# Kernel tuning notes

Hardware: AMD Instinct MI355X
Metric: run time of the kernel (lower is better)

The kernel has to match this reference:

```python
import jax, jax.numpy as jnp
import numpy as np

B, N, C = 32, 3136, 512
H = W = 56           # h = w = sqrt(n)
NUM_HEADS = 8
HEAD_DIM = C // NUM_HEADS
AGENT_NUM = 49
POOL = 7             # int(sqrt(agent_num))
SCALE = HEAD_DIM ** -0.5


def setup_inputs() -> dict:
    key = jax.random.key(0)
    ks = jax.random.split(key, 6)
    return {
        "x": jax.random.normal(ks[0], (B, N, C), dtype=jnp.float32),
        "qkv_w": jax.random.normal(ks[1], (3 * C, C), dtype=jnp.float32) * 0.02,
        "proj_w": jax.random.normal(ks[2], (C, C), dtype=jnp.float32) * 0.02,
        "proj_b": jax.random.normal(ks[3], (C,), dtype=jnp.float32) * 0.02,
        "dwc_w": jax.random.normal(ks[4], (C, 1, 3, 3), dtype=jnp.float32) * 0.02,
        "dwc_b": jax.random.normal(ks[5], (C,), dtype=jnp.float32) * 0.02,
    }


def reference(x, qkv_w, proj_w, proj_b, dwc_w, dwc_b):
    b, n, c = x.shape
    # qkv projection (no bias)
    qkv = jnp.einsum('bnc,dc->bnd', x, qkv_w).reshape(b, n, 3, c)
    q, k, v = qkv[:, :, 0], qkv[:, :, 1], qkv[:, :, 2]  # each (b, n, c)

    # adaptive avg pool q -> agent tokens (b, agent_num, c); 56/7 = stride 8
    s = H // POOL
    agent = q.reshape(b, POOL, s, POOL, s, c).mean(axis=(2, 4)).reshape(b, AGENT_NUM, c)

    # split heads: (b, heads, seq, head_dim)
    qh = q.reshape(b, n, NUM_HEADS, HEAD_DIM).transpose(0, 2, 1, 3)
    kh = k.reshape(b, n, NUM_HEADS, HEAD_DIM).transpose(0, 2, 1, 3)
    vh = v.reshape(b, n, NUM_HEADS, HEAD_DIM).transpose(0, 2, 1, 3)
    ah = agent.reshape(b, AGENT_NUM, NUM_HEADS, HEAD_DIM).transpose(0, 2, 1, 3)

    # agent aggregation: softmax((agent*scale) @ k^T) @ v -> (b, h, agent, d)
    agent_attn = jax.nn.softmax(jnp.einsum('bhad,bhnd->bhan', ah * SCALE, kh), axis=-1)
    agent_v = jnp.einsum('bhan,bhnd->bhad', agent_attn, vh)

    # query broadcast: softmax((q*scale) @ agent^T) @ agent_v -> (b, h, n, d)
    q_attn = jax.nn.softmax(jnp.einsum('bhnd,bhad->bhna', qh * SCALE, ah), axis=-1)
    out = jnp.einsum('bhna,bhad->bhnd', q_attn, agent_v)
    out = out.transpose(0, 2, 1, 3).reshape(b, n, c)

    # depthwise conv residual on v (NCHW)
    v_img = v.reshape(b, H, W, c).transpose(0, 3, 1, 2)
    dwc = jax.lax.conv_general_dilated(
        v_img, dwc_w, window_strides=(1, 1), padding=((1, 1), (1, 1)),
        dimension_numbers=('NCHW', 'OIHW', 'NCHW'), feature_group_count=c)
    dwc = dwc + dwc_b[None, :, None, None]
    out = out + dwc.transpose(0, 2, 3, 1).reshape(b, n, c)

    # output projection
    return jnp.einsum('bnc,dc->bnd', out, proj_w) + proj_b
```

## Files before the change

### kernel.cpp

```cpp
#include <hip/hip_runtime.h>

#define B_SZ 32
#define N_TOK 3136
#define C_DIM 512
#define H_IMG 56
#define NUM_HEADS 8
#define HEAD_DIM 64
#define AGENT_NUM 49
#define SCALE 0.125f
#define M_ROWS (B_SZ * N_TOK)
#define N_SPLIT 7

typedef __bf16 bf16x8 __attribute__((ext_vector_type(8)));
typedef float f32x4 __attribute__((ext_vector_type(4)));
typedef unsigned short u16x8 __attribute__((ext_vector_type(8)));
typedef unsigned int u32x4 __attribute__((ext_vector_type(4)));

static __device__ __forceinline__ unsigned short f2bf(float f) {
    unsigned int u = __float_as_uint(f);
    unsigned int r = (u + 0x7fffu + ((u >> 16) & 1u)) >> 16;
    return (unsigned short)r;
}
static __device__ __forceinline__ float bf2f(unsigned short u) {
    return __uint_as_float(((unsigned int)u) << 16);
}
static __device__ __forceinline__ void load_lds16(const unsigned short* g, unsigned short* l) {
    __builtin_amdgcn_global_load_lds(
        (const __attribute__((address_space(1))) unsigned int*)g,
        (__attribute__((address_space(3))) unsigned int*)l, 16, 0, 0);
}

__global__ __launch_bounds__(256) void cast_f32_bf16(
    const float* __restrict__ in, unsigned short* __restrict__ out)
{
    long i = (long)blockIdx.x * 256 + threadIdx.x;
    float4 f = ((const float4*)in)[i];
    ushort4 u;
    u.x = f2bf(f.x); u.y = f2bf(f.y); u.z = f2bf(f.z); u.w = f2bf(f.w);
    ((ushort4*)out)[i] = u;
}

__global__ __launch_bounds__(256) void mfma_qkv_bf(
    const unsigned short* __restrict__ Ab, const unsigned short* __restrict__ Wb,
    float* __restrict__ qO, unsigned short* __restrict__ kO,
    unsigned short* __restrict__ vO)
{
    __shared__ __align__(16) unsigned short Asm[2][128 * 32];
    __shared__ __align__(16) unsigned short Bsm[2][128 * 32];

    const int NWG  = (M_ROWS / 128) * 12;
    const int PERX = NWG >> 3;
    const int bid = blockIdx.x;
    const int l = (bid & 7) * PERX + (bid >> 3);
    const int m0 = (l / 12) * 128, n0 = (l % 12) * 128;

    const int tid = threadIdx.x;
    const int lane = tid & 63, wave = tid >> 6;
    const int wm = wave >> 1, wn = wave & 1;

    f32x4 acc[4][4];
#pragma unroll
    for (int i = 0; i < 4; i++)
#pragma unroll
        for (int j = 0; j < 4; j++) {
            f32x4 z = {0.f, 0.f, 0.f, 0.f};
            acc[i][j] = z;
        }

    const unsigned short* aP0 = Ab + (long)(m0 + (tid >> 2)) * 512 + (tid & 3) * 8;
    const unsigned short* aP1 = aP0 + (long)64 * 512;
    const unsigned short* bP0 = Wb + (long)(n0 + (tid >> 2)) * 512 + (tid & 3) * 8;
    const unsigned short* bP1 = bP0 + (long)64 * 512;
    const int stA0 = wave * 512;
    const int stA1 = wave * 512 + 2048;

    const int fr = lane & 15, fq = lane >> 4;
    const int fOff = fq * 8;

    load_lds16(aP0, Asm[0] + stA0);
    load_lds16(aP1, Asm[0] + stA1);
    load_lds16(bP0, Bsm[0] + stA0);
    load_lds16(bP1, Bsm[0] + stA1);
    __syncthreads();

    int cur = 0;
    for (int step = 0; step < 16; ++step) {
        if (step < 15) {
            const int k0 = (step + 1) * 32;
            load_lds16(aP0 + k0, Asm[cur ^ 1] + stA0);
            load_lds16(aP1 + k0, Asm[cur ^ 1] + stA1);
            load_lds16(bP0 + k0, Bsm[cur ^ 1] + stA0);
            load_lds16(bP1 + k0, Bsm[cur ^ 1] + stA1);
        }
        const unsigned short* aF = Asm[cur] + (wm * 64 + fr) * 32 + fOff;
        const unsigned short* bF = Bsm[cur] + (wn * 64 + fr) * 32 + fOff;
        bf16x8 af[4], bfr[4];
#pragma unroll
        for (int i = 0; i < 4; i++) af[i]  = *(const bf16x8*)(aF + i * 16 * 32);
#pragma unroll
        for (int j = 0; j < 4; j++) bfr[j] = *(const bf16x8*)(bF + j * 16 * 32);
#pragma unroll
        for (int i = 0; i < 4; i++)
#pragma unroll
            for (int j = 0; j < 4; j++)
                acc[i][j] = __builtin_amdgcn_mfma_f32_16x16x32_bf16(
                    af[i], bfr[j], acc[i][j], 0, 0, 0);
        __syncthreads();
        cur ^= 1;
    }

    const int seg = n0 >> 9;
#pragma unroll
    for (int i = 0; i < 4; i++) {
        int rbase = m0 + wm * 64 + i * 16 + fq * 4;
#pragma unroll
        for (int j = 0; j < 4; j++) {
            int col  = n0 + wn * 64 + j * 16 + fr;
            int nloc = col - seg * 512;
#pragma unroll
            for (int r = 0; r < 4; r++) {
                long m = rbase + r;
                float val = acc[i][j][r];
                if (seg == 0)      qO[m * 512 + nloc] = val;
                else if (seg == 1) kO[m * 512 + nloc] = f2bf(val);
                else               vO[m * 512 + nloc] = f2bf(val);
            }
        }
    }
}

__global__ __launch_bounds__(256) void mfma_qkv(
    const float* __restrict__ A, const unsigned short* __restrict__ Wb,
    float* __restrict__ qO, unsigned short* __restrict__ kO,
    unsigned short* __restrict__ vO)
{
    __shared__ __align__(16) unsigned short Asm[128 * 32];
    __shared__ __align__(16) unsigned short Bsm[128 * 32];

    const int m0 = blockIdx.x * 128, n0 = blockIdx.y * 128;
    const int tid = threadIdx.x;
    const int lane = tid & 63, wave = tid >> 6;
    const int wm = wave >> 1, wn = wave & 1;

    f32x4 acc[4][4];
#pragma unroll
    for (int i = 0; i < 4; i++)
#pragma unroll
        for (int j = 0; j < 4; j++) {
            f32x4 z = {0.f, 0.f, 0.f, 0.f};
            acc[i][j] = z;
        }

    const int arow = tid >> 1, acol = (tid & 1) * 16;
    const float* aP = A + (long)(m0 + arow) * 512 + acol;
    unsigned short* aD = Asm + arow * 32 + acol;

    const unsigned short* bP0 = Wb + (long)(n0 + (tid >> 2)) * 512 + (tid & 3) * 8;
    const unsigned short* bP1 = bP0 + (long)64 * 512;
    unsigned short* bD0 = Bsm + (tid >> 6) * 512;
    unsigned short* bD1 = bD0 + 4 * 512;

    const int fr = lane & 15, fq = lane >> 4;
    const unsigned short* aF = Asm + (wm * 64 + fr) * 32 + fq * 8;
    const unsigned short* bF = Bsm + (wn * 64 + fr) * 32 + fq * 8;

    for (int k0 = 0; k0 < 512; k0 += 32) {
        load_lds16(bP0 + k0, bD0);
        load_lds16(bP1 + k0, bD1);
        float4 f0 = *(const float4*)(aP + k0 + 0);
        float4 f1 = *(const float4*)(aP + k0 + 4);
        float4 f2 = *(const float4*)(aP + k0 + 8);
        float4 f3 = *(const float4*)(aP + k0 + 12);
        ushort4 u0, u1, u2, u3;
        u0.x = f2bf(f0.x); u0.y = f2bf(f0.y); u0.z = f2bf(f0.z); u0.w = f2bf(f0.w);
        u1.x = f2bf(f1.x); u1.y = f2bf(f1.y); u1.z = f2bf(f1.z); u1.w = f2bf(f1.w);
        u2.x = f2bf(f2.x); u2.y = f2bf(f2.y); u2.z = f2bf(f2.z); u2.w = f2bf(f2.w);
        u3.x = f2bf(f3.x); u3.y = f2bf(f3.y); u3.z = f2bf(f3.z); u3.w = f2bf(f3.w);
        *(ushort4*)(aD + 0)  = u0;
        *(ushort4*)(aD + 4)  = u1;
        *(ushort4*)(aD + 8)  = u2;
        *(ushort4*)(aD + 12) = u3;
        __syncthreads();

        bf16x8 af[4], bfr[4];
#pragma unroll
        for (int i = 0; i < 4; i++) af[i]  = *(const bf16x8*)(aF + i * 16 * 32);
#pragma unroll
        for (int j = 0; j < 4; j++) bfr[j] = *(const bf16x8*)(bF + j * 16 * 32);
#pragma unroll
        for (int i = 0; i < 4; i++)
#pragma unroll
            for (int j = 0; j < 4; j++)
                acc[i][j] = __builtin_amdgcn_mfma_f32_16x16x32_bf16(
                    af[i], bfr[j], acc[i][j], 0, 0, 0);
        __syncthreads();
    }

    const int seg = n0 >> 9;
#pragma unroll
    for (int i = 0; i < 4; i++) {
        int rbase = m0 + wm * 64 + i * 16 + fq * 4;
#pragma unroll
        for (int j = 0; j < 4; j++) {
            int col  = n0 + wn * 64 + j * 16 + fr;
            int nloc = col - seg * 512;
#pragma unroll
            for (int r = 0; r < 4; r++) {
                long m = rbase + r;
                float val = acc[i][j][r];
                if (seg == 0)      qO[m * 512 + nloc] = val;
                else if (seg == 1) kO[m * 512 + nloc] = f2bf(val);
                else               vO[m * 512 + nloc] = f2bf(val);
            }
        }
    }
}

__global__ __launch_bounds__(256) void mfma_proj(
    const unsigned short* __restrict__ Ab, const unsigned short* __restrict__ Wb,
    const float* __restrict__ bias, float* __restrict__ C)
{
    __shared__ __align__(16) unsigned short Asm[2][128 * 32];
    __shared__ __align__(16) unsigned short Bsm[2][128 * 32];

    const int NWG  = (M_ROWS / 128) * 4;
    const int PERX = NWG >> 3;
    const int bid = blockIdx.x;
    const int l = (bid & 7) * PERX + (bid >> 3);
    const int m0 = (l >> 2) * 128, n0 = (l & 3) * 128;

    const int tid = threadIdx.x;
    const int lane = tid & 63, wave = tid >> 6;
    const int wm = wave >> 1, wn = wave & 1;

    f32x4 acc[4][4];
#pragma unroll
    for (int i = 0; i < 4; i++)
#pragma unroll
        for (int j = 0; j < 4; j++) {
            f32x4 z = {0.f, 0.f, 0.f, 0.f};
            acc[i][j] = z;
        }

    const unsigned short* aP0 = Ab + (long)(m0 + (tid >> 2)) * 512 + (tid & 3) * 8;
    const unsigned short* aP1 = aP0 + (long)64 * 512;
    const unsigned short* bP0 = Wb + (long)(n0 + (tid >> 2)) * 512 + (tid & 3) * 8;
    const unsigned short* bP1 = bP0 + (long)64 * 512;
    const int stA0 = wave * 512;
    const int stA1 = wave * 512 + 2048;

    const int fr = lane & 15, fq = lane >> 4;
    const int fOff = fq * 8;

    load_lds16(aP0, Asm[0] + stA0);
    load_lds16(aP1, Asm[0] + stA1);
    load_lds16(bP0, Bsm[0] + stA0);
    load_lds16(bP1, Bsm[0] + stA1);
    __syncthreads();

    int cur = 0;
    for (int step = 0; step < 16; ++step) {
        if (step < 15) {
            const int k0 = (step + 1) * 32;
            load_lds16(aP0 + k0, Asm[cur ^ 1] + stA0);
            load_lds16(aP1 + k0, Asm[cur ^ 1] + stA1);
            load_lds16(bP0 + k0, Bsm[cur ^ 1] + stA0);
            load_lds16(bP1 + k0, Bsm[cur ^ 1] + stA1);
        }
        const unsigned short* aF = Asm[cur] + (wm * 64 + fr) * 32 + fOff;
        const unsigned short* bF = Bsm[cur] + (wn * 64 + fr) * 32 + fOff;
        bf16x8 af[4], bfr[4];
#pragma unroll
        for (int i = 0; i < 4; i++) af[i]  = *(const bf16x8*)(aF + i * 16 * 32);
#pragma unroll
        for (int j = 0; j < 4; j++) bfr[j] = *(const bf16x8*)(bF + j * 16 * 32);
#pragma unroll
        for (int i = 0; i < 4; i++)
#pragma unroll
            for (int j = 0; j < 4; j++)
                acc[i][j] = __builtin_amdgcn_mfma_f32_16x16x32_bf16(
                    af[i], bfr[j], acc[i][j], 0, 0, 0);
        __syncthreads();
        cur ^= 1;
    }

#pragma unroll
    for (int i = 0; i < 4; i++) {
        int rbase = m0 + wm * 64 + i * 16 + fq * 4;
#pragma unroll
        for (int j = 0; j < 4; j++) {
            int col = n0 + wn * 64 + j * 16 + fr;
            float bv = bias[col];
#pragma unroll
            for (int r = 0; r < 4; r++)
                C[(long)(rbase + r) * 512 + col] = acc[i][j][r] + bv;
        }
    }
}

__global__ __launch_bounds__(256) void pool_q(
    const float* __restrict__ q, float* __restrict__ agent)
{
    int blk = blockIdx.x;
    int half = blk & 1;
    int a = (blk >> 1) % AGENT_NUM;
    int b = blk / (2 * AGENT_NUM);
    int c = half * 256 + threadIdx.x;
    int pa = a / 7, pb = a % 7;
    const float* base = q + (long)b * N_TOK * 512 + c;
    float s = 0.f;
#pragma unroll
    for (int i = 0; i < 8; i++) {
        int rowbase = (pa * 8 + i) * H_IMG + pb * 8;
#pragma unroll
        for (int j = 0; j < 8; j++)
            s += base[(long)(rowbase + j) * 512];
    }
    agent[((long)b * AGENT_NUM + a) * 512 + c] = s * (1.f / 64.f);
}

__global__ __launch_bounds__(256) void agent_attn_mfma(
    const unsigned short* __restrict__ kO, const unsigned short* __restrict__ vO,
    const float* __restrict__ agent,
    float* __restrict__ macc, float* __restrict__ mpart, float* __restrict__ lpart)
{
    __shared__ __align__(16) unsigned short Ksm[64 * 64];
    __shared__ __align__(16) unsigned short Vsm[64 * 64];
    __shared__ __align__(16) unsigned short Psm[4 * 16 * 64];

    const int blk = blockIdx.x;
    const int s = blk % N_SPLIT;
    const int bh = blk / N_SPLIT;
    const int b = bh >> 3, h = bh & 7;
    const int tid = threadIdx.x;
    const int lane = tid & 63, w = tid >> 6;
    const int fr = lane & 15, fq = lane >> 4;

    bf16x8 afA[2];
    {
        int a = w * 16 + fr;
        const float* ap = agent + ((long)b * AGENT_NUM + a) * 512 + h * 64 + fq * 8;
#pragma unroll
        for (int kk = 0; kk < 2; kk++) {
            union { bf16x8 v; unsigned short u[8]; } cv;
#pragma unroll
            for (int e = 0; e < 8; e++) cv.u[e] = 0;
            if (a < AGENT_NUM) {
                float4 f0 = *(const float4*)(ap + kk * 32);
                float4 f1 = *(const float4*)(ap + kk * 32 + 4);
                cv.u[0] = f2bf(f0.x * SCALE); cv.u[1] = f2bf(f0.y * SCALE);
                cv.u[2] = f2bf(f0.z * SCALE); cv.u[3] = f2bf(f0.w * SCALE);
                cv.u[4] = f2bf(f1.x * SCALE); cv.u[5] = f2bf(f1.y * SCALE);
                cv.u[6] = f2bf(f1.z * SCALE); cv.u[7] = f2bf(f1.w * SCALE);
            }
            afA[kk] = cv.v;
        }
    }

    const unsigned short* kg = kO + (long)b * N_TOK * 512 + h * 64;
    const unsigned short* vg = vO + (long)b * N_TOK * 512 + h * 64;
    const int krow = tid >> 2, kcc = tid & 3;
    char* kdst0 = (char*)Ksm + krow * 128 + (((kcc * 2)     ^ (krow & 7)) * 16);
    char* kdst1 = (char*)Ksm + krow * 128 + (((kcc * 2 + 1) ^ (krow & 7)) * 16);
    const int vtp = tid & 31, vd0 = (tid >> 5) * 8;

    const int cs0 = ((fq)     ^ (fr & 7)) * 16;
    const int cs1 = ((4 + fq) ^ (fr & 7)) * 16;
    char* plb = (char*)Psm + w * 2048;

    f32x4 accO[4];
#pragma unroll
    for (int dj = 0; dj < 4; dj++) {
        f32x4 z = {0.f, 0.f, 0.f, 0.f};
        accO[dj] = z;
    }
    float m_a = -1e30f, l_a = 0.f;

    const int nstart = s * (N_TOK / N_SPLIT);
    for (int t = 0; t < 7; t++) {
        const int n0 = nstart + t * 64;
        __syncthreads();
        {
            const unsigned short* src = kg + (long)(n0 + krow) * 512 + kcc * 16;
            u32x4 d0 = *(const u32x4*)(src);
            u32x4 d1 = *(const u32x4*)(src + 8);
            *(u32x4*)kdst0 = d0;
            *(u32x4*)kdst1 = d1;
        }
        {
            const unsigned short* sv = vg + (long)(n0 + vtp * 2) * 512 + vd0;
            u16x8 v0 = *(const u16x8*)(sv);
            u16x8 v1 = *(const u16x8*)(sv + 512);
#pragma unroll
            for (int j = 0; j < 8; j++) {
                unsigned int val = (unsigned int)v0[j] | ((unsigned int)v1[j] << 16);
                *(unsigned int*)((char*)Vsm + (vd0 + j) * 128
                                 + (((vtp >> 2) ^ j) * 16) + (vtp & 3) * 4) = val;
            }
        }
        __syncthreads();

        f32x4 sacc[4];
#pragma unroll
        for (int it = 0; it < 4; it++) {
            f32x4 z = {0.f, 0.f, 0.f, 0.f};
            sacc[it] = z;
        }
#pragma unroll
        for (int it = 0; it < 4; it++) {
            bf16x8 kf0 = *(const bf16x8*)((char*)Ksm + it * 2048 + fr * 128 + cs0);
            bf16x8 kf1 = *(const bf16x8*)((char*)Ksm + it * 2048 + fr * 128 + cs1);
            sacc[it] = __builtin_amdgcn_mfma_f32_16x16x32_bf16(kf0, afA[0], sacc[it], 0, 0, 0);
            sacc[it] = __builtin_amdgcn_mfma_f32_16x16x32_bf16(kf1, afA[1], sacc[it], 0, 0, 0);
        }

        float mloc = -1e30f;
#pragma unroll
        for (int it = 0; it < 4; it++)
#pragma unroll
            for (int r = 0; r < 4; r++) mloc = fmaxf(mloc, sacc[it][r]);
        mloc = fmaxf(mloc, __shfl_xor(mloc, 16));
        mloc = fmaxf(mloc, __shfl_xor(mloc, 32));
        float mnew = fmaxf(m_a, mloc);
        float alpha = __expf(m_a - mnew);
        float p[4][4];
        float ss = 0.f;
#pragma unroll
        for (int it = 0; it < 4; it++)
#pragma unroll
            for (int r = 0; r < 4; r++) {
                float pv = __expf(sacc[it][r] - mnew);
                p[it][r] = pv;
                ss += pv;
            }
        ss += __shfl_xor(ss, 16);
        ss += __shfl_xor(ss, 32);
        l_a = l_a * alpha + ss;
        m_a = mnew;

#pragma unroll
        for (int it = 0; it < 4; it++)
#pragma unroll
            for (int pr = 0; pr < 2; pr++) {
                unsigned int u = (unsigned int)f2bf(p[it][pr * 2])
                               | ((unsigned int)f2bf(p[it][pr * 2 + 1]) << 16);
                *(unsigned int*)(plb + fr * 128
                    + (((it * 2 + (fq >> 1)) ^ (fr & 7)) * 16)
                    + (fq & 1) * 8 + pr * 4) = u;
            }

        float alr[4];
#pragma unroll
        for (int r = 0; r < 4; r++)
            alr[r] = __shfl(alpha, ((lane >> 4) << 2) + r);
#pragma unroll
        for (int dj = 0; dj < 4; dj++)
#pragma unroll
            for (int r = 0; r < 4; r++) accO[dj][r] *= alr[r];

        bf16x8 pf0 = *(const bf16x8*)(plb + fr * 128 + cs0);
        bf16x8 pf1 = *(const bf16x8*)(plb + fr * 128 + cs1);
#pragma unroll
        for (int dj = 0; dj < 4; dj++) {
            bf16x8 vf0 = *(const bf16x8*)((char*)Vsm + dj * 2048 + fr * 128 + cs0);
            bf16x8 vf1 = *(const bf16x8*)((char*)Vsm + dj * 2048 + fr * 128 + cs1);
            accO[dj] = __builtin_amdgcn_mfma_f32_16x16x32_bf16(pf0, vf0, accO[dj], 0, 0, 0);
            accO[dj] = __builtin_amdgcn_mfma_f32_16x16x32_bf16(pf1, vf1, accO[dj], 0, 0, 0);
        }
    }

    float* mob = macc + (long)blk * (AGENT_NUM * 64);
#pragma unroll
    for (int dj = 0; dj < 4; dj++)
#pragma unroll
        for (int r = 0; r < 4; r++) {
            int a = w * 16 + fq * 4 + r;
            if (a < AGENT_NUM)
                mob[a * 64 + dj * 16 + fr] = accO[dj][r];
        }
    if (fq == 0) {
        int a = w * 16 + fr;
        if (a < AGENT_NUM) {
            mpart[(long)blk * AGENT_NUM + a] = m_a;
            lpart[(long)blk * AGENT_NUM + a] = l_a;
        }
    }
}

__global__ __launch_bounds__(256) void agent_attn_combine(
    const float* __restrict__ macc, const float* __restrict__ mpart,
    const float* __restrict__ lpart, float* __restrict__ agent_v)
{
    int bh = blockIdx.x;
    int tid = threadIdx.x;
    __shared__ float E[AGENT_NUM * N_SPLIT];
    __shared__ float Linv[AGENT_NUM];

    if (tid < AGENT_NUM) {
        float mx = -1e30f;
        for (int s = 0; s < N_SPLIT; s++)
            mx = fmaxf(mx, mpart[((long)bh * N_SPLIT + s) * AGENT_NUM + tid]);
        float l = 0.f;
        for (int s = 0; s < N_SPLIT; s++) {
            float e = __expf(mpart[((long)bh * N_SPLIT + s) * AGENT_NUM + tid] - mx);
            E[tid * N_SPLIT + s] = e;
            l += e * lpart[((long)bh * N_SPLIT + s) * AGENT_NUM + tid];
        }
        Linv[tid] = 1.f / l;
    }
    __syncthreads();

    for (int idx = tid; idx < AGENT_NUM * 64; idx += 256) {
        int a = idx >> 6;
        float acc = 0.f;
        for (int s = 0; s < N_SPLIT; s++)
            acc += E[a * N_SPLIT + s] *
                   macc[((long)bh * N_SPLIT + s) * (AGENT_NUM * 64) + idx];
        agent_v[(long)bh * (AGENT_NUM * 64) + idx] = acc * Linv[a];
    }
}

__global__ __launch_bounds__(256) void q_attn(
    float* __restrict__ q, const float* __restrict__ agent,
    const float* __restrict__ agent_v)
{
    int chunk = blockIdx.x, h = blockIdx.y, b = blockIdx.z;
    int tid = threadIdx.x;

    __shared__ float ah[AGENT_NUM * 64];
    __shared__ float av[AGENT_NUM * 64];
    for (int idx = tid; idx < AGENT_NUM * 64; idx += 256) {
        int a = idx >> 6, d = idx & 63;
        ah[idx] = agent[((long)b * AGENT_NUM + a) * 512 + h * 64 + d];
        av[idx] = agent_v[((long)b * 8 + h) * (AGENT_NUM * 64) + idx];
    }
    __syncthreads();

    int n = chunk * 256 + tid;
    if (n >= N_TOK) return;

    float* qrow = q + ((long)b * N_TOK + n) * 512 + h * 64;
    float4 q4[16];
#pragma unroll
    for (int i = 0; i < 16; i++) q4[i] = *(float4*)(qrow + i * 4);

    float sc[AGENT_NUM];
#pragma unroll
    for (int a = 0; a < AGENT_NUM; a++) {
        const float* ap = ah + a * 64;
        float s = 0.f;
#pragma unroll
        for (int i = 0; i < 16; i++) {
            s += q4[i].x * ap[i * 4 + 0] + q4[i].y * ap[i * 4 + 1]
               + q4[i].z * ap[i * 4 + 2] + q4[i].w * ap[i * 4 + 3];
        }
        sc[a] = s * SCALE;
    }
    float mx = sc[0];
#pragma unroll
    for (int a = 1; a < AGENT_NUM; a++) mx = fmaxf(mx, sc[a]);
    float sum = 0.f;
#pragma unroll
    for (int a = 0; a < AGENT_NUM; a++) { sc[a] = __expf(sc[a] - mx); sum += sc[a]; }
    float inv = 1.f / sum;

#pragma unroll
    for (int d4 = 0; d4 < 16; d4++) {
        float4 o = make_float4(0.f, 0.f, 0.f, 0.f);
#pragma unroll
        for (int a = 0; a < AGENT_NUM; a++) {
            float p = sc[a];
            const float* vp = av + a * 64 + d4 * 4;
            o.x += p * vp[0]; o.y += p * vp[1];
            o.z += p * vp[2]; o.w += p * vp[3];
        }
        o.x *= inv; o.y *= inv; o.z *= inv; o.w *= inv;
        *(float4*)(qrow + d4 * 4) = o;
    }
}

__global__ __launch_bounds__(256) void dwc_fuse(
    const unsigned short* __restrict__ vO, const float* __restrict__ w,
    const float* __restrict__ bias, const float* __restrict__ attn,
    unsigned short* __restrict__ outb)
{
    __shared__ float ws2[64 * 73];
    for (int i = threadIdx.x; i < 512 * 9; i += 256) {
        int c = i / 9, k = i - c * 9;
        ws2[(c >> 3) * 73 + k * 8 + (c & 7)] = w[i];
    }
    __syncthreads();

    long flat = (long)blockIdx.x * 256 + threadIdx.x;
    int cg = (int)(flat & 63);
    int c8 = cg << 3;
    long row = flat >> 6;
    int n = (int)(row % N_TOK);
    int b = (int)(row / N_TOK);
    int y = n / H_IMG, x = n - y * H_IMG;

    const unsigned short* vb = vO + (long)b * N_TOK * 512 + c8;
    const float* wb = ws2 + cg * 73;

    float acc[8];
    float4 bv0 = *(const float4*)(bias + c8);
    float4 bv1 = *(const float4*)(bias + c8 + 4);
    acc[0] = bv0.x; acc[1] = bv0.y; acc[2] = bv0.z; acc[3] = bv0.w;
    acc[4] = bv1.x; acc[5] = bv1.y; acc[6] = bv1.z; acc[7] = bv1.w;

#pragma unroll
    for (int dy = 0; dy < 3; dy++) {
        int yy = y + dy - 1;
        if (yy < 0 || yy >= H_IMG) continue;
#pragma unroll
        for (int dx = 0; dx < 3; dx++) {
            int xx = x + dx - 1;
            if (xx < 0 || xx >= H_IMG) continue;
            const unsigned short* vp = vb + (long)(yy * H_IMG + xx) * 512;
            ushort4 u0 = *(const ushort4*)(vp);
            ushort4 u1 = *(const ushort4*)(vp + 4);
            const float* wk = wb + (dy * 3 + dx) * 8;
            acc[0] += wk[0] * bf2f(u0.x);
            acc[1] += wk[1] * bf2f(u0.y);
            acc[2] += wk[2] * bf2f(u0.z);
            acc[3] += wk[3] * bf2f(u0.w);
            acc[4] += wk[4] * bf2f(u1.x);
            acc[5] += wk[5] * bf2f(u1.y);
            acc[6] += wk[6] * bf2f(u1.z);
            acc[7] += wk[7] * bf2f(u1.w);
        }
    }

    const float* ap = attn + row * 512 + c8;
    float4 a0 = *(const float4*)(ap);
    float4 a1 = *(const float4*)(ap + 4);
    ushort4 o0, o1;
    o0.x = f2bf(a0.x + acc[0]); o0.y = f2bf(a0.y + acc[1]);
    o0.z = f2bf(a0.z + acc[2]); o0.w = f2bf(a0.w + acc[3]);
    o1.x = f2bf(a1.x + acc[4]); o1.y = f2bf(a1.y + acc[5]);
    o1.z = f2bf(a1.z + acc[6]); o1.w = f2bf(a1.w + acc[7]);

    unsigned short* op = outb + row * 512 + c8;
    *(ushort4*)(op)     = o0;
    *(ushort4*)(op + 4) = o1;
}

extern "C" void kernel_launch(void* const* d_in, const int* in_sizes, int n_in,
                              void* d_out, int out_size, void* d_ws, size_t ws_size,
                              hipStream_t stream)
{
    const float* x      = (const float*)d_in[0];
    const float* qkv_w  = (const float*)d_in[1];
    const float* proj_w = (const float*)d_in[2];
    const float* proj_b = (const float*)d_in[3];
    const float* dwc_w  = (const float*)d_in[4];
    const float* dwc_b  = (const float*)d_in[5];
    float* out = (float*)d_out;

    const long KV_ELEMS    = (long)M_ROWS * 512;
    const long QKVW_ELEMS  = 1536L * 512;
    const long PROJW_ELEMS = 512L * 512;
    const long AGENT_ELEMS = (long)B_SZ * AGENT_NUM * 512;
    const long AV_ELEMS    = (long)B_SZ * 8 * AGENT_NUM * 64;
    const long MACC_ELEMS  = (long)B_SZ * 8 * N_SPLIT * AGENT_NUM * 64;
    const long ML_ELEMS    = (long)B_SZ * 8 * N_SPLIT * AGENT_NUM;

    unsigned short* kbuf    = (unsigned short*)d_ws;
    unsigned short* vbuf    = kbuf + KV_ELEMS;
    unsigned short* qkv_wb  = vbuf + KV_ELEMS;
    unsigned short* proj_wb = qkv_wb + QKVW_ELEMS;
    float* agent   = (float*)(proj_wb + PROJW_ELEMS);
    float* agent_v = agent + AGENT_ELEMS;
    float* macc    = agent_v + AV_ELEMS;
    float* mpart   = macc + MACC_ELEMS;
    float* lpart   = mpart + ML_ELEMS;
    unsigned short* xb = (unsigned short*)(lpart + ML_ELEMS);

    size_t need_old = (size_t)(2 * KV_ELEMS + QKVW_ELEMS + PROJW_ELEMS) * 2
                    + (size_t)(AGENT_ELEMS + AV_ELEMS + MACC_ELEMS + 2 * ML_ELEMS) * 4;
    size_t need_new = need_old + (size_t)KV_ELEMS * 2;
    if (ws_size < need_old) return;
    const bool precast = (ws_size >= need_new);

    cast_f32_bf16<<<(unsigned)(QKVW_ELEMS / 1024), 256, 0, stream>>>(qkv_w, qkv_wb);
    cast_f32_bf16<<<(unsigned)(PROJW_ELEMS / 1024), 256, 0, stream>>>(proj_w, proj_wb);

    if (precast) {
        cast_f32_bf16<<<(unsigned)(KV_ELEMS / 1024), 256, 0, stream>>>(x, xb);
        mfma_qkv_bf<<<(M_ROWS / 128) * 12, 256, 0, stream>>>(
            xb, qkv_wb, out, kbuf, vbuf);
    } else {
        mfma_qkv<<<dim3(M_ROWS / 128, 12), 256, 0, stream>>>(
            x, qkv_wb, out, kbuf, vbuf);
    }

    pool_q<<<B_SZ * AGENT_NUM * 2, 256, 0, stream>>>(out, agent);

    agent_attn_mfma<<<B_SZ * 8 * N_SPLIT, 256, 0, stream>>>(
        kbuf, vbuf, agent, macc, mpart, lpart);
    agent_attn_combine<<<B_SZ * 8, 256, 0, stream>>>(macc, mpart, lpart, agent_v);

    q_attn<<<dim3((N_TOK + 255) / 256, 8, B_SZ), 256, 0, stream>>>(out, agent, agent_v);

    dwc_fuse<<<(unsigned)((long)M_ROWS * 64 / 256), 256, 0, stream>>>(
        vbuf, dwc_w, dwc_b, out, kbuf);

    mfma_proj<<<(M_ROWS / 128) * 4, 256, 0, stream>>>(kbuf, proj_wb, proj_b, out);
}
```

Baseline: 1.270 ms.

## Rewrite query-broadcast attention with bf16 MFMA per 64-token tile

Replaces the scalar fp32 q_attn kernel, where each thread computed 49 dot products and a 49-term weighted sum over LDS, with a single-wavefront MFMA kernel. The new kernel computes agent-by-query scores and the P·agent_v product with 16x16x32 bf16 MFMA instructions, and stages the probabilities through swizzled LDS. The aim is to cut the heavy scalar FMA and LDS traffic of the old kernel. The cost is bf16 rounding of q, agent, probabilities and agent_v, plus small 64-thread blocks with strided scalar output stores.

```diff
diff --git a/kernel.cpp b/kernel.cpp
--- a/kernel.cpp
+++ b/kernel.cpp
@@ -339,13 +339,13 @@
     bf16x8 afA[2];
     {
         int a = w * 16 + fr;
-        const float* ap = agent + ((long)b * AGENT_NUM + a) * 512 + h * 64 + fq * 8;
 #pragma unroll
         for (int kk = 0; kk < 2; kk++) {
             union { bf16x8 v; unsigned short u[8]; } cv;
 #pragma unroll
             for (int e = 0; e < 8; e++) cv.u[e] = 0;
             if (a < AGENT_NUM) {
+                const float* ap = agent + ((long)b * AGENT_NUM + a) * 512 + h * 64 + fq * 8;
                 float4 f0 = *(const float4*)(ap + kk * 32);
                 float4 f1 = *(const float4*)(ap + kk * 32 + 4);
                 cv.u[0] = f2bf(f0.x * SCALE); cv.u[1] = f2bf(f0.y * SCALE);
@@ -520,62 +520,158 @@
     }
 }
 
-__global__ __launch_bounds__(256) void q_attn(
+__global__ __launch_bounds__(64) void q_attn_mfma(
     float* __restrict__ q, const float* __restrict__ agent,
     const float* __restrict__ agent_v)
 {
-    int chunk = blockIdx.x, h = blockIdx.y, b = blockIdx.z;
-    int tid = threadIdx.x;
-
-    __shared__ float ah[AGENT_NUM * 64];
-    __shared__ float av[AGENT_NUM * 64];
-    for (int idx = tid; idx < AGENT_NUM * 64; idx += 256) {
-        int a = idx >> 6, d = idx & 63;
-        ah[idx] = agent[((long)b * AGENT_NUM + a) * 512 + h * 64 + d];
-        av[idx] = agent_v[((long)b * 8 + h) * (AGENT_NUM * 64) + idx];
-    }
-    __syncthreads();
-
-    int n = chunk * 256 + tid;
-    if (n >= N_TOK) return;
-
-    float* qrow = q + ((long)b * N_TOK + n) * 512 + h * 64;
-    float4 q4[16];
-#pragma unroll
-    for (int i = 0; i < 16; i++) q4[i] = *(float4*)(qrow + i * 4);
-
-    float sc[AGENT_NUM];
-#pragma unroll
-    for (int a = 0; a < AGENT_NUM; a++) {
-        const float* ap = ah + a * 64;
-        float s = 0.f;
-#pragma unroll
-        for (int i = 0; i < 16; i++) {
-            s += q4[i].x * ap[i * 4 + 0] + q4[i].y * ap[i * 4 + 1]
-               + q4[i].z * ap[i * 4 + 2] + q4[i].w * ap[i * 4 + 3];
-        }
-        sc[a] = s * SCALE;
-    }
-    float mx = sc[0];
-#pragma unroll
-    for (int a = 1; a < AGENT_NUM; a++) mx = fmaxf(mx, sc[a]);
-    float sum = 0.f;
-#pragma unroll
-    for (int a = 0; a < AGENT_NUM; a++) { sc[a] = __expf(sc[a] - mx); sum += sc[a]; }
-    float inv = 1.f / sum;
-
-#pragma unroll
-    for (int d4 = 0; d4 < 16; d4++) {
-        float4 o = make_float4(0.f, 0.f, 0.f, 0.f);
-#pragma unroll
-        for (int a = 0; a < AGENT_NUM; a++) {
-            float p = sc[a];
-            const float* vp = av + a * 64 + d4 * 4;
-            o.x += p * vp[0]; o.y += p * vp[1];
-            o.z += p * vp[2]; o.w += p * vp[3];
-        }
-        o.x *= inv; o.y *= inv; o.z *= inv; o.w *= inv;
-        *(float4*)(qrow + d4 * 4) = o;
+    __shared__ __align__(16) unsigned short Psm[64 * 64];
+
+    const int blk = blockIdx.x;
+    const int c = blk % 49;
+    const int bh = blk / 49;
+    const int b = bh >> 3, h = bh & 7;
+    const int lane = threadIdx.x;
+    const int fr = lane & 15, fq = lane >> 4;
+    const int q0 = c * 64;
+
+    bf16x8 agA[4][2];
+#pragma unroll
+    for (int i = 0; i < 4; i++) {
+        int a = i * 16 + fr;
+#pragma unroll
+        for (int kk = 0; kk < 2; kk++) {
+            union { bf16x8 v; unsigned short u[8]; } cv;
+#pragma unroll
+            for (int e = 0; e < 8; e++) cv.u[e] = 0;
+            if (a < AGENT_NUM) {
+                const float* ap = agent + ((long)b * AGENT_NUM + a) * 512 + h * 64 + fq * 8;
+                float4 f0 = *(const float4*)(ap + kk * 32);
+                float4 f1 = *(const float4*)(ap + kk * 32 + 4);
+                cv.u[0] = f2bf(f0.x * SCALE); cv.u[1] = f2bf(f0.y * SCALE);
+                cv.u[2] = f2bf(f0.z * SCALE); cv.u[3] = f2bf(f0.w * SCALE);
+                cv.u[4] = f2bf(f1.x * SCALE); cv.u[5] = f2bf(f1.y * SCALE);
+                cv.u[6] = f2bf(f1.z * SCALE); cv.u[7] = f2bf(f1.w * SCALE);
+            }
+            agA[i][kk] = cv.v;
+        }
+    }
+
+    bf16x8 qB[4][2];
+#pragma unroll
+    for (int jq = 0; jq < 4; jq++) {
+        const float* qp = q + ((long)b * N_TOK + q0 + jq * 16 + fr) * 512
+                        + h * 64 + fq * 8;
+#pragma unroll
+        for (int kk = 0; kk < 2; kk++) {
+            float4 f0 = *(const float4*)(qp + kk * 32);
+            float4 f1 = *(const float4*)(qp + kk * 32 + 4);
+            union { bf16x8 v; unsigned short u[8]; } cv;
+            cv.u[0] = f2bf(f0.x); cv.u[1] = f2bf(f0.y);
+            cv.u[2] = f2bf(f0.z); cv.u[3] = f2bf(f0.w);
+            cv.u[4] = f2bf(f1.x); cv.u[5] = f2bf(f1.y);
+            cv.u[6] = f2bf(f1.z); cv.u[7] = f2bf(f1.w);
+            qB[jq][kk] = cv.v;
+        }
+    }
+
+    f32x4 sacc[4][4];
+#pragma unroll
+    for (int i = 0; i < 4; i++)
+#pragma unroll
+        for (int jq = 0; jq < 4; jq++) {
+            f32x4 z = {0.f, 0.f, 0.f, 0.f};
+            sacc[i][jq] = z;
+        }
+#pragma unroll
+    for (int i = 0; i < 4; i++)
+#pragma unroll
+        for (int jq = 0; jq < 4; jq++) {
+            sacc[i][jq] = __builtin_amdgcn_mfma_f32_16x16x32_bf16(
+                agA[i][0], qB[jq][0], sacc[i][jq], 0, 0, 0);
+            sacc[i][jq] = __builtin_amdgcn_mfma_f32_16x16x32_bf16(
+                agA[i][1], qB[jq][1], sacc[i][jq], 0, 0, 0);
+        }
+
+#pragma unroll
+    for (int jq = 0; jq < 4; jq++)
+#pragma unroll
+        for (int r = 0; r < 4; r++)
+            if ((fq << 2) + r > 0) sacc[3][jq][r] = -1e30f;
+
+#pragma unroll
+    for (int jq = 0; jq < 4; jq++) {
+        float mx = -1e30f;
+#pragma unroll
+        for (int i = 0; i < 4; i++)
+#pragma unroll
+            for (int r = 0; r < 4; r++) mx = fmaxf(mx, sacc[i][jq][r]);
+        mx = fmaxf(mx, __shfl_xor(mx, 16));
+        mx = fmaxf(mx, __shfl_xor(mx, 32));
+        float ss = 0.f;
+#pragma unroll
+        for (int i = 0; i < 4; i++)
+#pragma unroll
+            for (int r = 0; r < 4; r++) {
+                float pv = __expf(sacc[i][jq][r] - mx);
+                sacc[i][jq][r] = pv;
+                ss += pv;
+            }
+        ss += __shfl_xor(ss, 16);
+        ss += __shfl_xor(ss, 32);
+        float inv = 1.f / ss;
+#pragma unroll
+        for (int i = 0; i < 4; i++)
+#pragma unroll
+            for (int r = 0; r < 4; r++) sacc[i][jq][r] *= inv;
+    }
+
+#pragma unroll
+    for (int jq = 0; jq < 4; jq++) {
+        char* prow = (char*)Psm + (jq * 16 + fr) * 128;
+#pragma unroll
+        for (int i = 0; i < 4; i++)
+#pragma unroll
+            for (int pr = 0; pr < 2; pr++) {
+                unsigned int u = (unsigned int)f2bf(sacc[i][jq][pr * 2])
+                               | ((unsigned int)f2bf(sacc[i][jq][pr * 2 + 1]) << 16);
+                *(unsigned int*)(prow
+                    + (((i * 2 + (fq >> 1)) ^ (fr & 7)) * 16)
+                    + (fq & 1) * 8 + pr * 4) = u;
+            }
+    }
+
+    const float* avb = agent_v + (long)bh * (AGENT_NUM * 64);
+    bf16x8 avB[4][2];
+#pragma unroll
+    for (int jd = 0; jd < 4; jd++)
+#pragma unroll
+        for (int kk = 0; kk < 2; kk++) {
+            union { bf16x8 v; unsigned short u[8]; } cv;
+#pragma unroll
+            for (int e = 0; e < 8; e++) {
+                int a = kk * 32 + fq * 8 + e;
+                cv.u[e] = (a < AGENT_NUM) ? f2bf(avb[a * 64 + jd * 16 + fr]) : 0;
+            }
+            avB[jd][kk] = cv.v;
+        }
+
+    const int cs0 = ((fq)     ^ (fr & 7)) * 16;
+    const int cs1 = ((4 + fq) ^ (fr & 7)) * 16;
+#pragma unroll
+    for (int iq = 0; iq < 4; iq++) {
+        char* prow = (char*)Psm + (iq * 16 + fr) * 128;
+        bf16x8 pf0 = *(const bf16x8*)(prow + cs0);
+        bf16x8 pf1 = *(const bf16x8*)(prow + cs1);
+        float* orow = q + ((long)b * N_TOK + q0 + iq * 16 + fq * 4) * 512 + h * 64;
+#pragma unroll
+        for (int jd = 0; jd < 4; jd++) {
+            f32x4 o = {0.f, 0.f, 0.f, 0.f};
+            o = __builtin_amdgcn_mfma_f32_16x16x32_bf16(pf0, avB[jd][0], o, 0, 0, 0);
+            o = __builtin_amdgcn_mfma_f32_16x16x32_bf16(pf1, avB[jd][1], o, 0, 0, 0);
+#pragma unroll
+            for (int r = 0; r < 4; r++)
+                orow[(long)r * 512 + jd * 16 + fr] = o[r];
+        }
     }
 }
 
@@ -700,7 +796,7 @@
         kbuf, vbuf, agent, macc, mpart, lpart);
     agent_attn_combine<<<B_SZ * 8, 256, 0, stream>>>(macc, mpart, lpart, agent_v);
 
-    q_attn<<<dim3((N_TOK + 255) / 256, 8, B_SZ), 256, 0, stream>>>(out, agent, agent_v);
+    q_attn_mfma<<<B_SZ * 8 * 49, 64, 0, stream>>>(out, agent, agent_v);
 
     dwc_fuse<<<(unsigned)((long)M_ROWS * 64 / 256), 256, 0, stream>>>(
         vbuf, dwc_w, dwc_b, out, kbuf);
```

Measured after the change: 1.145 ms. 9.9% less time.
